# Kernel tuning notes

Hardware: AMD Instinct MI355X
Metric: run time of the kernel (lower is better)

## Reference

```python
import jax, jax.numpy as jnp
import numpy as np

N, E, LE = 200000, 1000000, 1000000
ND, ED = 128, 128
EPS = 1e-5


def layer_norm(v, g, b):
    m = v.mean(-1, keepdims=True)
    var = ((v - m) ** 2).mean(-1, keepdims=True)
    return (v - m) * jax.lax.rsqrt(var + EPS) * g + b


def setup_inputs() -> dict:
    key = jax.random.key(0)
    ks = jax.random.split(key, 12)
    s = 0.02
    return {
        "x": jax.random.normal(ks[0], (N, ND), jnp.float32),
        "edge_attr": jax.random.normal(ks[1], (E, ED), jnp.float32),
        "lg_x": jax.random.normal(ks[2], (E, ED), jnp.float32),
        "lg_edge_attr": jax.random.normal(ks[3], (LE, 1), jnp.float32),
        "W_line": jax.random.normal(ks[4], (2 * ED + 1, ED), jnp.float32) * s,
        "b_line": jnp.zeros((ED,), jnp.float32),
        "W_gate": jax.random.normal(ks[5], (ED, ED), jnp.float32) * s,
        "b_gate": jnp.zeros((ED,), jnp.float32),
        "W_atom": jax.random.normal(ks[6], (ND + ED, ND), jnp.float32) * s,
        "b_atom": jnp.zeros((ND,), jnp.float32),
        "g_node": jnp.ones((ND,), jnp.float32),
        "beta_node": jnp.zeros((ND,), jnp.float32),
        "g_edge": jnp.ones((ED,), jnp.float32),
        "beta_edge": jnp.zeros((ED,), jnp.float32),
        "edge_index": jax.random.randint(ks[7], (2, E), 0, N, jnp.int64),
        "lg_edge_index": jax.random.randint(ks[8], (2, LE), 0, E, jnp.int64),
    }


def reference(x, edge_attr, lg_x, lg_edge_attr, W_line, b_line, W_gate, b_gate,
              W_atom, b_atom, g_node, beta_node, g_edge, beta_edge,
              edge_index, lg_edge_index):
    n_lg = lg_x.shape[0]  # == E (line-graph nodes are bonds)
    lg_src, lg_dst = lg_edge_index[0], lg_edge_index[1]
    # 1) LineGraphConv: gather-concat-MLP-scatter(mean)
    msg = jnp.concatenate([lg_x[lg_src], lg_x[lg_dst], lg_edge_attr], axis=-1)  # [LE, 2*ED+1]
    msg = jax.nn.silu(msg @ W_line + b_line)  # [LE, ED]
    agg_sum = jax.ops.segment_sum(msg, lg_dst, num_segments=n_lg)
    cnt = jax.ops.segment_sum(jnp.ones((lg_dst.shape[0], 1), msg.dtype), lg_dst, num_segments=n_lg)
    lg_x_new = lg_x + agg_sum / jnp.maximum(cnt, 1.0)  # scatter-mean, empty segs -> 0
    # 2) EdgeGateUpdate
    edge_attr_new = layer_norm(edge_attr + lg_x_new, g_edge, beta_edge)
    gate = jax.nn.sigmoid(edge_attr_new @ W_gate + b_gate)
    # 3) AtomGraphConv: gated scatter(sum) into atoms
    col = edge_index[1]
    agg = jax.ops.segment_sum(gate * edge_attr_new, col, num_segments=x.shape[0])  # [N, ED]
    h = jax.nn.silu(jnp.concatenate([x, agg], axis=-1) @ W_atom + b_atom)
    x_new = layer_norm(x + h, g_node, beta_node)
    return x_new, edge_attr_new, lg_x_new
```

## Files before the change

### kernel.cpp

```cpp
#include <hip/hip_runtime.h>


typedef __attribute__((ext_vector_type(8))) short s16x8;
typedef __attribute__((ext_vector_type(4))) float f32x4;

#define SCAN_CHUNK 2048

__device__ __forceinline__ short f2bf(float f) {
    unsigned u = __float_as_uint(f);
    u += 0x7FFF + ((u >> 16) & 1);
    return (short)(u >> 16);
}
__device__ __forceinline__ float bf2f(unsigned short h) {
    return __uint_as_float(((unsigned)h) << 16);
}
__device__ __forceinline__ s16x8 pack8(const float* v) {
    s16x8 r;
    #pragma unroll
    for (int j = 0; j < 8; ++j) r[j] = f2bf(v[j]);
    return r;
}

__global__ __launch_bounds__(256) void k_pack3(
    const float* __restrict__ Wl, const float* __restrict__ Wg,
    const float* __restrict__ Wa,
    short* __restrict__ Pl, short* __restrict__ Pg, short* __restrict__ Pa)
{
    int c = blockIdx.x * 256 + threadIdx.x;
    const float* W; short* P; int cc;
    if (c < 4096)       { W = Wl; P = Pl; cc = c; }
    else if (c < 6144)  { W = Wg; P = Pg; cc = c - 4096; }
    else if (c < 10240) { W = Wa; P = Pa; cc = c - 6144; }
    else return;
    int g = cc >> 7, col = cc & 127, k0 = g * 8;
    s16x8 v;
    #pragma unroll
    for (int j = 0; j < 8; ++j) v[j] = f2bf(W[(size_t)(k0 + j) * 128 + col]);
    ((s16x8*)P)[cc] = v;
}

__global__ __launch_bounds__(256) void k_cvt(const float* __restrict__ x,
                                             short* __restrict__ y, long n8) {
    long i = (long)blockIdx.x * 256 + threadIdx.x;
    const long stride = (long)gridDim.x * 256;
    for (; i < n8; i += stride) {
        float buf[8];
        *(float4*)&buf[0] = ((const float4*)x)[2 * i];
        *(float4*)&buf[4] = ((const float4*)x)[2 * i + 1];
        ((s16x8*)y)[i] = pack8(buf);
    }
}

__global__ __launch_bounds__(256) void k_hist2(
    const int* __restrict__ idx1, int* __restrict__ deg1, int n1,
    const int* __restrict__ idx2, int* __restrict__ deg2, int n2)
{
    int i = blockIdx.x * 256 + threadIdx.x;
    if (i < n1) atomicAdd(&deg1[idx1[i]], 1);
    if (i < n2) atomicAdd(&deg2[idx2[i]], 1);
}

__global__ __launch_bounds__(256) void k_scan_block2(
    const int* __restrict__ in1, int n1, int* __restrict__ out1, int* __restrict__ bsum1, int nb1,
    const int* __restrict__ in2, int n2, int* __restrict__ out2, int* __restrict__ bsum2)
{
    __shared__ int ts[256];
    int b = blockIdx.x;
    const int* in; int n; int* out; int* bsum;
    if (b < nb1) { in = in1; n = n1; out = out1; bsum = bsum1; }
    else         { in = in2; n = n2; out = out2; bsum = bsum2; b -= nb1; }
    const int t = threadIdx.x;
    const int base = b * SCAN_CHUNK + t * 8;
    int v[8]; int s = 0;
    #pragma unroll
    for (int i = 0; i < 8; ++i) { v[i] = (base + i < n) ? in[base + i] : 0; s += v[i]; }
    ts[t] = s;
    __syncthreads();
    int x = s;
    for (int off = 1; off < 256; off <<= 1) {
        int y = (t >= off) ? ts[t - off] : 0;
        __syncthreads();
        x += y; ts[t] = x;
        __syncthreads();
    }
    if (t == 255) bsum[b] = x;
    int run = x - s;
    #pragma unroll
    for (int i = 0; i < 8; ++i) {
        if (base + i < n) out[base + i] = run;
        run += v[i];
    }
}

__global__ void k_scan_bsum2(int* __restrict__ b1, int nb1,
                             int* __restrict__ b2, int nb2) {
    const int lane = threadIdx.x & 63;
    int* bsum = (threadIdx.x < 64) ? b1 : b2;
    const int nb  = (threadIdx.x < 64) ? nb1 : nb2;
    int carry = 0;
    for (int base = 0; base < nb; base += 64) {
        int i = base + lane;
        int v = (i < nb) ? bsum[i] : 0;
        int inc = v;
        #pragma unroll
        for (int off = 1; off < 64; off <<= 1) {
            int t = __shfl_up(inc, off);
            if (lane >= off) inc += t;
        }
        if (i < nb) bsum[i] = inc - v + carry;
        carry += __shfl(inc, 63);
    }
}

__global__ __launch_bounds__(256) void k_scan_add2(
    int* __restrict__ off1, const int* __restrict__ bsum1, int n1, int ne1,
    int* __restrict__ off2, const int* __restrict__ bsum2, int n2, int ne2)
{
    int i = blockIdx.x * 256 + threadIdx.x;
    if (i < n1) off1[i] += bsum1[i / SCAN_CHUNK];
    if (i < n2) off2[i] += bsum2[i / SCAN_CHUNK];
    if (i == 0) { off1[n1] = ne1; off2[n2] = ne2; }
}

__global__ __launch_bounds__(256) void k_fill_pos2(
    const int* __restrict__ idx1, const int* __restrict__ off1,
    int* __restrict__ cur1, int* __restrict__ pos1, int n1,
    const int* __restrict__ idx2, const int* __restrict__ off2,
    int* __restrict__ cur2, int* __restrict__ pos2, int n2)
{
    int i = blockIdx.x * 256 + threadIdx.x;
    if (i < n1) {
        int s = idx1[i];
        int p = atomicAdd(&cur1[s], 1);
        pos1[i] = off1[s] + p;
    }
    if (i < n2) {
        int s = idx2[i];
        int p = atomicAdd(&cur2[s], 1);
        pos2[i] = off2[s] + p;
    }
}

__global__ __launch_bounds__(256) void k_line_csr(
    const short* __restrict__ lgx_bf, const float* __restrict__ lg_ea,
    const short* __restrict__ Wp, const float* __restrict__ W_line,
    const float* __restrict__ b_line,
    const int* __restrict__ lg_src, const int* __restrict__ lg_dst,
    const int* __restrict__ pos_lg,
    short* __restrict__ msg, int LEn)
{
    __shared__ __align__(16) short sh[128][136];
    const int tid = threadIdx.x;
    const int ln = tid & 63, wv = tid >> 6;
    const int l15 = ln & 15, lhi = ln >> 4;
    const int eb = blockIdx.x * 128 + wv * 32;
    const s16x8* Bv = (const s16x8*)Wp;

    const short *sp[2], *dp[2];
    #pragma unroll
    for (int mt = 0; mt < 2; ++mt) {
        int e = eb + mt * 16 + l15;
        int ec = e < LEn ? e : LEn - 1;
        sp[mt] = lgx_bf + (size_t)lg_src[ec] * 128;
        dp[mt] = lgx_bf + (size_t)lg_dst[ec] * 128;
    }

    f32x4 acc[2][8];
    #pragma unroll
    for (int m = 0; m < 2; ++m)
        #pragma unroll
        for (int n = 0; n < 8; ++n) acc[m][n] = (f32x4){0.f, 0.f, 0.f, 0.f};

    #pragma unroll 2
    for (int kt = 0; kt < 8; ++kt) {
        int ko = (kt & 3) * 32 + lhi * 8;
        s16x8 a[2];
        #pragma unroll
        for (int mt = 0; mt < 2; ++mt)
            a[mt] = *(const s16x8*)(((kt < 4) ? sp[mt] : dp[mt]) + ko);
        const s16x8* brow = Bv + (size_t)(kt * 4 + lhi) * 128 + l15;
        #pragma unroll
        for (int nt = 0; nt < 8; ++nt) {
            s16x8 b = brow[nt * 16];
            acc[0][nt] = __builtin_amdgcn_mfma_f32_16x16x32_bf16(a[0], b, acc[0][nt], 0, 0, 0);
            acc[1][nt] = __builtin_amdgcn_mfma_f32_16x16x32_bf16(a[1], b, acc[1][nt], 0, 0, 0);
        }
    }

    float eav[2][4];
    #pragma unroll
    for (int mt = 0; mt < 2; ++mt)
        #pragma unroll
        for (int r = 0; r < 4; ++r) {
            int e = eb + mt * 16 + lhi * 4 + r;
            eav[mt][r] = lg_ea[e < LEn ? e : 0];
        }

    #pragma unroll
    for (int nt = 0; nt < 8; ++nt) {
        int col = nt * 16 + l15;
        float wl = W_line[(size_t)256 * 128 + col];
        float bs = b_line[col];
        #pragma unroll
        for (int mt = 0; mt < 2; ++mt)
            #pragma unroll
            for (int r = 0; r < 4; ++r) {
                float v = acc[mt][nt][r] + bs + wl * eav[mt][r];
                float s = v / (1.f + __expf(-v));
                sh[wv * 32 + mt * 16 + lhi * 4 + r][col] = f2bf(s);
            }
    }
    __syncthreads();
    #pragma unroll
    for (int i = 0; i < 8; ++i) {
        int c = tid + i * 256;
        int row = c >> 4, q = c & 15;
        int e = blockIdx.x * 128 + row;
        if (e < LEn) {
            int p = pos_lg[e];
            *(s16x8*)&msg[(size_t)p * 128 + q * 8] = *(const s16x8*)&sh[row][q * 8];
        }
    }
}

__global__ __launch_bounds__(256) void k_lg_edge_fused(
    const short* __restrict__ msg, const short* __restrict__ lgx_bf,
    const float* __restrict__ edge_attr, const int* __restrict__ off,
    const float* __restrict__ g_edge, const float* __restrict__ beta_edge,
    float* __restrict__ out_lg, float* __restrict__ out_edge,
    short* __restrict__ enew_bf, int En)
{
    const int wave = threadIdx.x >> 6, lane = threadIdx.x & 63;
    const int half = lane >> 5, l = lane & 31;
    const int e = blockIdx.x * 8 + wave * 2 + half;
    if (e >= En) return;
    const int o0 = off[e], o1 = off[e + 1];
    const int cnt = o1 - o0;
    const short* mbase = msg + (size_t)o0 * 128 + l * 4;
    float s0 = 0.f, s1 = 0.f, s2 = 0.f, s3 = 0.f;
    for (int j = 0; j < cnt; ++j) {
        ushort4 u = *(const ushort4*)(mbase + (size_t)j * 128);
        s0 += bf2f(u.x); s1 += bf2f(u.y); s2 += bf2f(u.z); s3 += bf2f(u.w);
    }
    const float inv = 1.f / fmaxf((float)cnt, 1.f);
    const size_t rb = (size_t)e * 128 + l * 4;
    ushort4 lxu = *(const ushort4*)&lgx_bf[rb];
    float l0 = fmaf(s0, inv, bf2f(lxu.x));
    float l1 = fmaf(s1, inv, bf2f(lxu.y));
    float l2 = fmaf(s2, inv, bf2f(lxu.z));
    float l3 = fmaf(s3, inv, bf2f(lxu.w));
    *(float4*)&out_lg[rb] = make_float4(l0, l1, l2, l3);

    float4 ea = *(const float4*)&edge_attr[rb];
    float t0 = ea.x + l0, t1 = ea.y + l1, t2 = ea.z + l2, t3 = ea.w + l3;
    float s = t0 + t1 + t2 + t3;
    float sq = t0 * t0 + t1 * t1 + t2 * t2 + t3 * t3;
    #pragma unroll
    for (int o = 16; o; o >>= 1) {
        s  += __shfl_xor(s, o);
        sq += __shfl_xor(sq, o);
    }
    float mean = s * (1.f / 128.f);
    float var  = sq * (1.f / 128.f) - mean * mean;
    float r = rsqrtf(var + 1e-5f);
    int j0 = l * 4;
    float4 gg = *(const float4*)&g_edge[j0];
    float4 bb = *(const float4*)&beta_edge[j0];
    float e0 = fmaf((t0 - mean) * r, gg.x, bb.x);
    float e1 = fmaf((t1 - mean) * r, gg.y, bb.y);
    float e2 = fmaf((t2 - mean) * r, gg.z, bb.z);
    float e3 = fmaf((t3 - mean) * r, gg.w, bb.w);
    *(float4*)&out_edge[rb] = make_float4(e0, e1, e2, e3);
    if (enew_bf) {
        ushort4 ub = make_ushort4((unsigned short)f2bf(e0), (unsigned short)f2bf(e1),
                                  (unsigned short)f2bf(e2), (unsigned short)f2bf(e3));
        *(ushort4*)&enew_bf[rb] = ub;
    }
}

__global__ __launch_bounds__(256) void k_lg_gather(
    const short* __restrict__ msg, const float* __restrict__ lg_x,
    const int* __restrict__ off, float* __restrict__ out_lg, int En)
{
    const int wave = threadIdx.x >> 6, lane = threadIdx.x & 63;
    const int e = blockIdx.x * 4 + wave;
    if (e >= En) return;
    const int o0 = off[e], o1 = off[e + 1];
    const int cnt = o1 - o0;
    const short* base = msg + (size_t)o0 * 128 + lane * 2;
    float s0 = 0.f, s1 = 0.f;
    for (int j = 0; j < cnt; ++j) {
        ushort2 u = *(const ushort2*)(base + (size_t)j * 128);
        s0 += bf2f(u.x); s1 += bf2f(u.y);
    }
    const float inv = 1.f / fmaxf((float)cnt, 1.f);
    const size_t rb = (size_t)e * 128 + lane * 2;
    float2 lx = *(const float2*)&lg_x[rb];
    *(float2*)&out_lg[rb] = make_float2(fmaf(s0, inv, lx.x), fmaf(s1, inv, lx.y));
}

__global__ __launch_bounds__(256) void k_edge_ln(
    const float* __restrict__ lnew, const float* __restrict__ edge_attr,
    const float* __restrict__ g_edge, const float* __restrict__ beta_edge,
    float* __restrict__ out_edge, int En)
{
    const int wave = threadIdx.x >> 6, lane = threadIdx.x & 63;
    const int e = blockIdx.x * 4 + wave;
    if (e >= En) return;
    const size_t rb = (size_t)e * 128 + lane * 2;
    float2 lv = *(const float2*)&lnew[rb];
    float2 ea = *(const float2*)&edge_attr[rb];
    float t0 = ea.x + lv.x, t1 = ea.y + lv.y;
    float s = t0 + t1, sq = t0 * t0 + t1 * t1;
    #pragma unroll
    for (int o = 32; o; o >>= 1) { s += __shfl_xor(s, o); sq += __shfl_xor(sq, o); }
    float mean = s * (1.f / 128.f);
    float var  = sq * (1.f / 128.f) - mean * mean;
    float r = rsqrtf(var + 1e-5f);
    int j0 = lane * 2;
    float o0 = (t0 - mean) * r * g_edge[j0]     + beta_edge[j0];
    float o1 = (t1 - mean) * r * g_edge[j0 + 1] + beta_edge[j0 + 1];
    *(float2*)&out_edge[rb] = make_float2(o0, o1);
}

template <bool BF>
__global__ __launch_bounds__(256) void k_gate_csr(
    const short* __restrict__ EinB, const float* __restrict__ EinF,
    const short* __restrict__ Wp, const float* __restrict__ bg,
    const int* __restrict__ pos_at, short* __restrict__ gated, int En)
{
    __shared__ __align__(16) short sh[128][136];
    const int tid = threadIdx.x;
    const int ln = tid & 63, wv = tid >> 6;
    const int l15 = ln & 15, lhi = ln >> 4;
    const int eb = blockIdx.x * 128 + wv * 32;
    const s16x8* Bv = (const s16x8*)Wp;

    int rowi[2];
    #pragma unroll
    for (int mt = 0; mt < 2; ++mt) {
        int e = eb + mt * 16 + l15;
        rowi[mt] = e < En ? e : En - 1;
    }

    f32x4 acc[2][8];
    #pragma unroll
    for (int m = 0; m < 2; ++m)
        #pragma unroll
        for (int n = 0; n < 8; ++n) acc[m][n] = (f32x4){0.f, 0.f, 0.f, 0.f};

    #pragma unroll 2
    for (int kt = 0; kt < 4; ++kt) {
        int ko = kt * 32 + lhi * 8;
        s16x8 a[2];
        #pragma unroll
        for (int mt = 0; mt < 2; ++mt) {
            if (BF) {
                a[mt] = *(const s16x8*)(EinB + (size_t)rowi[mt] * 128 + ko);
            } else {
                const float* p = EinF + (size_t)rowi[mt] * 128 + ko;
                float buf[8];
                *(float4*)&buf[0] = *(const float4*)p;
                *(float4*)&buf[4] = *(const float4*)(p + 4);
                a[mt] = pack8(buf);
            }
        }
        const s16x8* brow = Bv + (size_t)(kt * 4 + lhi) * 128 + l15;
        #pragma unroll
        for (int nt = 0; nt < 8; ++nt) {
            s16x8 b = brow[nt * 16];
            acc[0][nt] = __builtin_amdgcn_mfma_f32_16x16x32_bf16(a[0], b, acc[0][nt], 0, 0, 0);
            acc[1][nt] = __builtin_amdgcn_mfma_f32_16x16x32_bf16(a[1], b, acc[1][nt], 0, 0, 0);
        }
    }

    #pragma unroll
    for (int nt = 0; nt < 8; ++nt) {
        int col = nt * 16 + l15;
        float bs = bg[col];
        #pragma unroll
        for (int mt = 0; mt < 2; ++mt)
            #pragma unroll
            for (int r = 0; r < 4; ++r) {
                int e = eb + mt * 16 + lhi * 4 + r;
                int ec = e < En ? e : En - 1;
                float g = 1.f / (1.f + __expf(-(acc[mt][nt][r] + bs)));
                float ev = BF ? bf2f(((const unsigned short*)EinB)[(size_t)ec * 128 + col])
                              : EinF[(size_t)ec * 128 + col];
                sh[wv * 32 + mt * 16 + lhi * 4 + r][col] = f2bf(g * ev);
            }
    }
    __syncthreads();
    #pragma unroll
    for (int i = 0; i < 8; ++i) {
        int c = tid + i * 256;
        int row = c >> 4, q = c & 15;
        int e = blockIdx.x * 128 + row;
        if (e < En) {
            int p = pos_at[e];
            *(s16x8*)&gated[(size_t)p * 128 + q * 8] = *(const s16x8*)&sh[row][q * 8];
        }
    }
}

template <bool BF_OUT>
__global__ __launch_bounds__(256) void k_atom_gather(
    const short* __restrict__ gated, const int* __restrict__ off,
    float* __restrict__ aggf, short* __restrict__ aggb, int Nn)
{
    const int wave = threadIdx.x >> 6, lane = threadIdx.x & 63;
    const int half = lane >> 5, l = lane & 31;
    const int n = blockIdx.x * 8 + wave * 2 + half;
    if (n >= Nn) return;
    const int o0 = off[n], o1 = off[n + 1];
    const int cnt = o1 - o0;
    const short* base = gated + (size_t)o0 * 128 + l * 4;
    float s0 = 0.f, s1 = 0.f, s2 = 0.f, s3 = 0.f;
    for (int j = 0; j < cnt; ++j) {
        ushort4 u = *(const ushort4*)(base + (size_t)j * 128);
        s0 += bf2f(u.x); s1 += bf2f(u.y); s2 += bf2f(u.z); s3 += bf2f(u.w);
    }
    const size_t rb = (size_t)n * 128 + l * 4;
    if (BF_OUT) {
        ushort4 ub = make_ushort4((unsigned short)f2bf(s0), (unsigned short)f2bf(s1),
                                  (unsigned short)f2bf(s2), (unsigned short)f2bf(s3));
        *(ushort4*)&aggb[rb] = ub;
    } else {
        *(float4*)&aggf[rb] = make_float4(s0, s1, s2, s3);
    }
}

template <bool AGGBF>
__global__ __launch_bounds__(256) void k_atom_mfma(
    const float* __restrict__ x, const float* __restrict__ aggf,
    const short* __restrict__ aggb,
    const short* __restrict__ Wp, const float* __restrict__ ba,
    const float* __restrict__ gn, const float* __restrict__ bn,
    float* __restrict__ out, int Nn)
{
    const int tid = threadIdx.x;
    const int ln = tid & 63, wv = tid >> 6;
    const int l15 = ln & 15, lhi = ln >> 4;
    const int nb = blockIdx.x * 128 + wv * 32;
    const s16x8* Bv = (const s16x8*)Wp;

    const float* xp[2];
    size_t nc[2];
    #pragma unroll
    for (int mt = 0; mt < 2; ++mt) {
        int n = nb + mt * 16 + l15;
        nc[mt] = (size_t)(n < Nn ? n : Nn - 1) * 128;
        xp[mt] = x + nc[mt];
    }

    f32x4 acc[2][8];
    #pragma unroll
    for (int m = 0; m < 2; ++m)
        #pragma unroll
        for (int n = 0; n < 8; ++n) acc[m][n] = (f32x4){0.f, 0.f, 0.f, 0.f};

    #pragma unroll 2
    for (int kt = 0; kt < 8; ++kt) {
        int ko = (kt & 3) * 32 + lhi * 8;
        s16x8 a[2];
        #pragma unroll
        for (int mt = 0; mt < 2; ++mt) {
            if (kt < 4) {
                const float* p = xp[mt] + ko;
                float buf[8];
                *(float4*)&buf[0] = *(const float4*)p;
                *(float4*)&buf[4] = *(const float4*)(p + 4);
                a[mt] = pack8(buf);
            } else if (AGGBF) {
                a[mt] = *(const s16x8*)(aggb + nc[mt] + ko);
            } else {
                const float* p = aggf + nc[mt] + ko;
                float buf[8];
                *(float4*)&buf[0] = *(const float4*)p;
                *(float4*)&buf[4] = *(const float4*)(p + 4);
                a[mt] = pack8(buf);
            }
        }
        const s16x8* brow = Bv + (size_t)(kt * 4 + lhi) * 128 + l15;
        #pragma unroll
        for (int nt = 0; nt < 8; ++nt) {
            s16x8 b = brow[nt * 16];
            acc[0][nt] = __builtin_amdgcn_mfma_f32_16x16x32_bf16(a[0], b, acc[0][nt], 0, 0, 0);
            acc[1][nt] = __builtin_amdgcn_mfma_f32_16x16x32_bf16(a[1], b, acc[1][nt], 0, 0, 0);
        }
    }

    #pragma unroll
    for (int mt = 0; mt < 2; ++mt)
        #pragma unroll
        for (int r = 0; r < 4; ++r) {
            int n = nb + mt * 16 + lhi * 4 + r;
            size_t nr = (size_t)(n < Nn ? n : 0) * 128;
            float s = 0.f, sq = 0.f;
            #pragma unroll
            for (int nt = 0; nt < 8; ++nt) {
                int col = nt * 16 + l15;
                float v = acc[mt][nt][r] + ba[col];
                float h = v / (1.f + __expf(-v));
                float t = x[nr + col] + h;
                acc[mt][nt][r] = t;
                s += t; sq += t * t;
            }
            #pragma unroll
            for (int off = 8; off; off >>= 1) {
                s  += __shfl_xor(s, off);
                sq += __shfl_xor(sq, off);
            }
            float mean = s * (1.f / 128.f);
            float var  = sq * (1.f / 128.f) - mean * mean;
            float rstd = rsqrtf(var + 1e-5f);
            if (n < Nn) {
                #pragma unroll
                for (int nt = 0; nt < 8; ++nt) {
                    int col = nt * 16 + l15;
                    float o = (acc[mt][nt][r] - mean) * rstd * gn[col] + bn[col];
                    out[(size_t)n * 128 + col] = o;
                }
            }
        }
}

extern "C" void kernel_launch(void* const* d_in, const int* in_sizes, int n_in,
                              void* d_out, int out_size, void* d_ws, size_t ws_size,
                              hipStream_t stream) {
    const float* x          = (const float*)d_in[0];
    const float* edge_attr  = (const float*)d_in[1];
    const float* lg_x       = (const float*)d_in[2];
    const float* lg_ea      = (const float*)d_in[3];
    const float* W_line     = (const float*)d_in[4];
    const float* b_line     = (const float*)d_in[5];
    const float* W_gate     = (const float*)d_in[6];
    const float* b_gate     = (const float*)d_in[7];
    const float* W_atom     = (const float*)d_in[8];
    const float* b_atom     = (const float*)d_in[9];
    const float* g_node     = (const float*)d_in[10];
    const float* beta_node  = (const float*)d_in[11];
    const float* g_edge     = (const float*)d_in[12];
    const float* beta_edge  = (const float*)d_in[13];
    const int*   edge_index    = (const int*)d_in[14];
    const int*   lg_edge_index = (const int*)d_in[15];

    const int Nn  = in_sizes[0] / 128;
    const int En  = in_sizes[1] / 128;
    const int LEn = in_sizes[3];

    float* out_x    = (float*)d_out;
    float* out_edge = out_x + (size_t)Nn * 128;
    float* out_lg   = out_edge + (size_t)En * 128;

    const int* lg_src = lg_edge_index;
    const int* lg_dst = lg_edge_index + LEn;
    const int* col    = edge_index + En;

    short* wp_line = (short*)d_ws;
    short* wp_gate = wp_line + 32768;
    short* wp_atom = wp_gate + 16384;
    int* ip = (int*)(wp_atom + 32768);
    int* off_lg  = ip;  ip += En + 1;
    int* deg_lg  = ip;  ip += En;
    int* cur_lg  = ip;  ip += En;
    int* pos_lg  = ip;  ip += LEn;
    int* bsum_lg = ip;  ip += 1024;
    int* off_at  = ip;  ip += Nn + 1;
    int* deg_at  = ip;  ip += Nn;
    int* cur_at  = ip;  ip += Nn;
    int* pos_at  = ip;  ip += En;
    int* bsum_at = ip;  ip += 1024;
    short* lgx_bf = (short*)(((uintptr_t)ip + 15) & ~(uintptr_t)15);
    short* bufA   = lgx_bf + (size_t)En * 128;
    short* agg_bf = bufA + (size_t)En * 128;
    const size_t need_B = ((uintptr_t)bufA) - (uintptr_t)d_ws;
    const size_t need_A = ((uintptr_t)(agg_bf + (size_t)Nn * 128)) - (uintptr_t)d_ws;
    const bool tierA = ws_size >= need_A;

    hipMemsetAsync(deg_lg, 0, (size_t)En * 8, stream);
    hipMemsetAsync(deg_at, 0, (size_t)Nn * 8, stream);

    k_pack3<<<40, 256, 0, stream>>>(W_line, W_gate, W_atom, wp_line, wp_gate, wp_atom);
    k_cvt<<<2048, 256, 0, stream>>>(lg_x, lgx_bf, (long)En * 16);

    const int nmax = LEn > En ? LEn : En;
    k_hist2<<<(nmax + 255) / 256, 256, 0, stream>>>(lg_dst, deg_lg, LEn, col, deg_at, En);
    const int nb_lg = (En + SCAN_CHUNK - 1) / SCAN_CHUNK;
    const int nb_at = (Nn + SCAN_CHUNK - 1) / SCAN_CHUNK;
    k_scan_block2<<<nb_lg + nb_at, 256, 0, stream>>>(
        deg_lg, En, off_lg, bsum_lg, nb_lg, deg_at, Nn, off_at, bsum_at);
    k_scan_bsum2<<<1, 128, 0, stream>>>(bsum_lg, nb_lg, bsum_at, nb_at);
    const int sa_max = En > Nn ? En : Nn;
    k_scan_add2<<<(sa_max + 255) / 256, 256, 0, stream>>>(
        off_lg, bsum_lg, En, LEn, off_at, bsum_at, Nn, En);
    k_fill_pos2<<<(nmax + 255) / 256, 256, 0, stream>>>(
        lg_dst, off_lg, cur_lg, pos_lg, LEn, col, off_at, cur_at, pos_at, En);

    if (tierA) {
        short* msg = bufA;
        k_line_csr<<<(LEn + 127) / 128, 256, 0, stream>>>(
            lgx_bf, lg_ea, wp_line, W_line, b_line, lg_src, lg_dst, pos_lg, msg, LEn);
        short* enew_bf = lgx_bf;
        k_lg_edge_fused<<<(En + 7) / 8, 256, 0, stream>>>(
            msg, lgx_bf, edge_attr, off_lg, g_edge, beta_edge,
            out_lg, out_edge, enew_bf, En);
        short* gated = bufA;
        k_gate_csr<true><<<(En + 127) / 128, 256, 0, stream>>>(
            enew_bf, nullptr, wp_gate, b_gate, pos_at, gated, En);
        k_atom_gather<true><<<(Nn + 7) / 8, 256, 0, stream>>>(
            gated, off_at, nullptr, agg_bf, Nn);
        k_atom_mfma<true><<<(Nn + 127) / 128, 256, 0, stream>>>(
            x, nullptr, agg_bf, wp_atom, b_atom, g_node, beta_node, out_x, Nn);
    } else {
        short* msg = (short*)out_edge;
        k_line_csr<<<(LEn + 127) / 128, 256, 0, stream>>>(
            lgx_bf, lg_ea, wp_line, W_line, b_line, lg_src, lg_dst, pos_lg, msg, LEn);
        k_lg_gather<<<(En + 3) / 4, 256, 0, stream>>>(msg, lg_x, off_lg, out_lg, En);
        k_edge_ln<<<(En + 3) / 4, 256, 0, stream>>>(
            out_lg, edge_attr, g_edge, beta_edge, out_edge, En);
        short* gated = lgx_bf;
        k_gate_csr<false><<<(En + 127) / 128, 256, 0, stream>>>(
            nullptr, out_edge, wp_gate, b_gate, pos_at, gated, En);
        k_atom_gather<false><<<(Nn + 7) / 8, 256, 0, stream>>>(
            gated, off_at, out_x, nullptr, Nn);
        k_atom_mfma<false><<<(Nn + 127) / 128, 256, 0, stream>>>(
            x, out_x, nullptr, wp_atom, b_atom, g_node, beta_node, out_x, Nn);
    }
}
```

Measured before the change: 1.536 ms.

## Process line-graph edges in destination-sorted order and merge prep kernels

The line-graph message kernel now walks edges in CSR (destination-sorted) order through a permutation array. Message rows are written contiguously instead of scattered to computed positions, and consecutive edges share destination rows, which should help gather locality. The gate kernel stages its bf16 edge tile in shared memory with coalesced loads instead of strided per-element global reads. The weight packing, lg_x conversion and histogram kernels are merged into one launch to cut launch overhead. In exchange, source and attribute reads become indirect through the permutation, and the fill kernel now does a scattered write of the permutation.

```diff
diff --git a/kernel.cpp b/kernel.cpp
--- a/kernel.cpp
+++ b/kernel.cpp
@@ -21,43 +21,42 @@
     return r;
 }
 
-__global__ __launch_bounds__(256) void k_pack3(
+__global__ __launch_bounds__(256) void k_prep(
     const float* __restrict__ Wl, const float* __restrict__ Wg,
     const float* __restrict__ Wa,
-    short* __restrict__ Pl, short* __restrict__ Pg, short* __restrict__ Pa)
-{
-    int c = blockIdx.x * 256 + threadIdx.x;
-    const float* W; short* P; int cc;
-    if (c < 4096)       { W = Wl; P = Pl; cc = c; }
-    else if (c < 6144)  { W = Wg; P = Pg; cc = c - 4096; }
-    else if (c < 10240) { W = Wa; P = Pa; cc = c - 6144; }
-    else return;
-    int g = cc >> 7, col = cc & 127, k0 = g * 8;
-    s16x8 v;
-    #pragma unroll
-    for (int j = 0; j < 8; ++j) v[j] = f2bf(W[(size_t)(k0 + j) * 128 + col]);
-    ((s16x8*)P)[cc] = v;
-}
-
-__global__ __launch_bounds__(256) void k_cvt(const float* __restrict__ x,
-                                             short* __restrict__ y, long n8) {
-    long i = (long)blockIdx.x * 256 + threadIdx.x;
-    const long stride = (long)gridDim.x * 256;
-    for (; i < n8; i += stride) {
-        float buf[8];
-        *(float4*)&buf[0] = ((const float4*)x)[2 * i];
-        *(float4*)&buf[4] = ((const float4*)x)[2 * i + 1];
-        ((s16x8*)y)[i] = pack8(buf);
-    }
-}
-
-__global__ __launch_bounds__(256) void k_hist2(
+    short* __restrict__ Pl, short* __restrict__ Pg, short* __restrict__ Pa,
+    const float* __restrict__ lgx, short* __restrict__ lgx_bf, long n8,
     const int* __restrict__ idx1, int* __restrict__ deg1, int n1,
-    const int* __restrict__ idx2, int* __restrict__ deg2, int n2)
-{
-    int i = blockIdx.x * 256 + threadIdx.x;
-    if (i < n1) atomicAdd(&deg1[idx1[i]], 1);
-    if (i < n2) atomicAdd(&deg2[idx2[i]], 1);
+    const int* __restrict__ idx2, int* __restrict__ deg2, int n2,
+    int cvtBlocks)
+{
+    const int b = blockIdx.x;
+    if (b < 40) {
+        int c = b * 256 + threadIdx.x;
+        const float* W; short* P; int cc;
+        if (c < 4096)       { W = Wl; P = Pl; cc = c; }
+        else if (c < 6144)  { W = Wg; P = Pg; cc = c - 4096; }
+        else if (c < 10240) { W = Wa; P = Pa; cc = c - 6144; }
+        else return;
+        int g = cc >> 7, col = cc & 127, k0 = g * 8;
+        s16x8 v;
+        #pragma unroll
+        for (int j = 0; j < 8; ++j) v[j] = f2bf(W[(size_t)(k0 + j) * 128 + col]);
+        ((s16x8*)P)[cc] = v;
+    } else if (b < 40 + cvtBlocks) {
+        long i = (long)(b - 40) * 256 + threadIdx.x;
+        const long stride = (long)cvtBlocks * 256;
+        for (; i < n8; i += stride) {
+            float buf[8];
+            *(float4*)&buf[0] = ((const float4*)lgx)[2 * i];
+            *(float4*)&buf[4] = ((const float4*)lgx)[2 * i + 1];
+            ((s16x8*)lgx_bf)[i] = pack8(buf);
+        }
+    } else {
+        int i = (b - 40 - cvtBlocks) * 256 + threadIdx.x;
+        if (i < n1) atomicAdd(&deg1[idx1[i]], 1);
+        if (i < n2) atomicAdd(&deg2[idx2[i]], 1);
+    }
 }
 
 __global__ __launch_bounds__(256) void k_scan_block2(
@@ -122,9 +121,9 @@
     if (i == 0) { off1[n1] = ne1; off2[n2] = ne2; }
 }
 
-__global__ __launch_bounds__(256) void k_fill_pos2(
+__global__ __launch_bounds__(256) void k_fill2(
     const int* __restrict__ idx1, const int* __restrict__ off1,
-    int* __restrict__ cur1, int* __restrict__ pos1, int n1,
+    int* __restrict__ cur1, int* __restrict__ perm1, int n1,
     const int* __restrict__ idx2, const int* __restrict__ off2,
     int* __restrict__ cur2, int* __restrict__ pos2, int n2)
 {
@@ -132,7 +131,7 @@
     if (i < n1) {
         int s = idx1[i];
         int p = atomicAdd(&cur1[s], 1);
-        pos1[i] = off1[s] + p;
+        perm1[off1[s] + p] = i;
     }
     if (i < n2) {
         int s = idx2[i];
@@ -146,23 +145,26 @@
     const short* __restrict__ Wp, const float* __restrict__ W_line,
     const float* __restrict__ b_line,
     const int* __restrict__ lg_src, const int* __restrict__ lg_dst,
-    const int* __restrict__ pos_lg,
+    const int* __restrict__ perm_lg,
     short* __restrict__ msg, int LEn)
 {
     __shared__ __align__(16) short sh[128][136];
     const int tid = threadIdx.x;
     const int ln = tid & 63, wv = tid >> 6;
     const int l15 = ln & 15, lhi = ln >> 4;
-    const int eb = blockIdx.x * 128 + wv * 32;
+    const int pb = blockIdx.x * 128 + wv * 32;
     const s16x8* Bv = (const s16x8*)Wp;
 
     const short *sp[2], *dp[2];
+    int ev_e[2];
     #pragma unroll
     for (int mt = 0; mt < 2; ++mt) {
-        int e = eb + mt * 16 + l15;
-        int ec = e < LEn ? e : LEn - 1;
-        sp[mt] = lgx_bf + (size_t)lg_src[ec] * 128;
-        dp[mt] = lgx_bf + (size_t)lg_dst[ec] * 128;
+        int p = pb + mt * 16 + l15;
+        int pc = p < LEn ? p : LEn - 1;
+        int e = perm_lg[pc];
+        ev_e[mt] = e;
+        sp[mt] = lgx_bf + (size_t)lg_src[e] * 128;
+        dp[mt] = lgx_bf + (size_t)lg_dst[e] * 128;
     }
 
     f32x4 acc[2][8];
@@ -192,8 +194,9 @@
     for (int mt = 0; mt < 2; ++mt)
         #pragma unroll
         for (int r = 0; r < 4; ++r) {
-            int e = eb + mt * 16 + lhi * 4 + r;
-            eav[mt][r] = lg_ea[e < LEn ? e : 0];
+            int p = pb + mt * 16 + lhi * 4 + r;
+            int pc = p < LEn ? p : LEn - 1;
+            eav[mt][r] = lg_ea[perm_lg[pc]];
         }
 
     #pragma unroll
@@ -215,11 +218,9 @@
     for (int i = 0; i < 8; ++i) {
         int c = tid + i * 256;
         int row = c >> 4, q = c & 15;
-        int e = blockIdx.x * 128 + row;
-        if (e < LEn) {
-            int p = pos_lg[e];
+        int p = blockIdx.x * 128 + row;
+        if (p < LEn)
             *(s16x8*)&msg[(size_t)p * 128 + q * 8] = *(const s16x8*)&sh[row][q * 8];
-        }
     }
 }
 
@@ -336,6 +337,18 @@
     const int eb = blockIdx.x * 128 + wv * 32;
     const s16x8* Bv = (const s16x8*)Wp;
 
+    if (BF) {
+        #pragma unroll
+        for (int i = 0; i < 8; ++i) {
+            int c = tid + i * 256;
+            int row = c >> 4, q = c & 15;
+            int e = blockIdx.x * 128 + row;
+            int ec = e < En ? e : En - 1;
+            *(s16x8*)&sh[row][q * 8] = *(const s16x8*)&EinB[(size_t)ec * 128 + q * 8];
+        }
+        __syncthreads();
+    }
+
     int rowi[2];
     #pragma unroll
     for (int mt = 0; mt < 2; ++mt) {
@@ -382,12 +395,13 @@
         for (int mt = 0; mt < 2; ++mt)
             #pragma unroll
             for (int r = 0; r < 4; ++r) {
+                int row = wv * 32 + mt * 16 + lhi * 4 + r;
                 int e = eb + mt * 16 + lhi * 4 + r;
                 int ec = e < En ? e : En - 1;
                 float g = 1.f / (1.f + __expf(-(acc[mt][nt][r] + bs)));
-                float ev = BF ? bf2f(((const unsigned short*)EinB)[(size_t)ec * 128 + col])
+                float ev = BF ? bf2f((unsigned short)sh[row][col])
                               : EinF[(size_t)ec * 128 + col];
-                sh[wv * 32 + mt * 16 + lhi * 4 + r][col] = f2bf(g * ev);
+                sh[row][col] = f2bf(g * ev);
             }
     }
     __syncthreads();
@@ -564,7 +578,7 @@
     int* off_lg  = ip;  ip += En + 1;
     int* deg_lg  = ip;  ip += En;
     int* cur_lg  = ip;  ip += En;
-    int* pos_lg  = ip;  ip += LEn;
+    int* perm_lg = ip;  ip += LEn;
     int* bsum_lg = ip;  ip += 1024;
     int* off_at  = ip;  ip += Nn + 1;
     int* deg_at  = ip;  ip += Nn;
@@ -574,18 +588,20 @@
     short* lgx_bf = (short*)(((uintptr_t)ip + 15) & ~(uintptr_t)15);
     short* bufA   = lgx_bf + (size_t)En * 128;
     short* agg_bf = bufA + (size_t)En * 128;
-    const size_t need_B = ((uintptr_t)bufA) - (uintptr_t)d_ws;
     const size_t need_A = ((uintptr_t)(agg_bf + (size_t)Nn * 128)) - (uintptr_t)d_ws;
     const bool tierA = ws_size >= need_A;
 
     hipMemsetAsync(deg_lg, 0, (size_t)En * 8, stream);
     hipMemsetAsync(deg_at, 0, (size_t)Nn * 8, stream);
 
-    k_pack3<<<40, 256, 0, stream>>>(W_line, W_gate, W_atom, wp_line, wp_gate, wp_atom);
-    k_cvt<<<2048, 256, 0, stream>>>(lg_x, lgx_bf, (long)En * 16);
-
     const int nmax = LEn > En ? LEn : En;
-    k_hist2<<<(nmax + 255) / 256, 256, 0, stream>>>(lg_dst, deg_lg, LEn, col, deg_at, En);
+    const int cvtBlocks = 2048;
+    const int histBlocks = (nmax + 255) / 256;
+    k_prep<<<40 + cvtBlocks + histBlocks, 256, 0, stream>>>(
+        W_line, W_gate, W_atom, wp_line, wp_gate, wp_atom,
+        lg_x, lgx_bf, (long)En * 16,
+        lg_dst, deg_lg, LEn, col, deg_at, En, cvtBlocks);
+
     const int nb_lg = (En + SCAN_CHUNK - 1) / SCAN_CHUNK;
     const int nb_at = (Nn + SCAN_CHUNK - 1) / SCAN_CHUNK;
     k_scan_block2<<<nb_lg + nb_at, 256, 0, stream>>>(
@@ -594,13 +610,13 @@
     const int sa_max = En > Nn ? En : Nn;
     k_scan_add2<<<(sa_max + 255) / 256, 256, 0, stream>>>(
         off_lg, bsum_lg, En, LEn, off_at, bsum_at, Nn, En);
-    k_fill_pos2<<<(nmax + 255) / 256, 256, 0, stream>>>(
-        lg_dst, off_lg, cur_lg, pos_lg, LEn, col, off_at, cur_at, pos_at, En);
+    k_fill2<<<(nmax + 255) / 256, 256, 0, stream>>>(
+        lg_dst, off_lg, cur_lg, perm_lg, LEn, col, off_at, cur_at, pos_at, En);
 
     if (tierA) {
         short* msg = bufA;
         k_line_csr<<<(LEn + 127) / 128, 256, 0, stream>>>(
-            lgx_bf, lg_ea, wp_line, W_line, b_line, lg_src, lg_dst, pos_lg, msg, LEn);
+            lgx_bf, lg_ea, wp_line, W_line, b_line, lg_src, lg_dst, perm_lg, msg, LEn);
         short* enew_bf = lgx_bf;
         k_lg_edge_fused<<<(En + 7) / 8, 256, 0, stream>>>(
             msg, lgx_bf, edge_attr, off_lg, g_edge, beta_edge,
@@ -615,7 +631,7 @@
     } else {
         short* msg = (short*)out_edge;
         k_line_csr<<<(LEn + 127) / 128, 256, 0, stream>>>(
-            lgx_bf, lg_ea, wp_line, W_line, b_line, lg_src, lg_dst, pos_lg, msg, LEn);
+            lgx_bf, lg_ea, wp_line, W_line, b_line, lg_src, lg_dst, perm_lg, msg, LEn);
         k_lg_gather<<<(En + 3) / 4, 256, 0, stream>>>(msg, lg_x, off_lg, out_lg, En);
         k_edge_ln<<<(En + 3) / 4, 256, 0, stream>>>(
             out_lg, edge_attr, g_edge, beta_edge, out_edge, En);
```

Result: faster. 1.449 ms (-5.7%).
